# Kernel tuning notes

Measured on AMD Instinct MI355X. Metric: run time of the kernel, lower is better.

## Reference

```python
import jax, jax.numpy as jnp
import numpy as np

N = 16_777_216  # number of draft tokens / cache slots
ACCEPT_PROB = 0.7


def setup_inputs() -> dict:
    key = jax.random.key(0)
    k1, k2, k3 = jax.random.split(key, 3)
    idx = jax.random.randint(k1, (N,), 0, N, dtype=jnp.int64)
    keep = jax.random.uniform(k2, (N,)) < ACCEPT_PROB
    # rejected slots are marked -1, as in the original kernel
    accept_index = jnp.where(keep, idx, jnp.int64(-1))
    out_cache_loc = jax.random.normal(k3, (N,), dtype=jnp.float32)
    return {"accept_index": accept_index, "out_cache_loc": out_cache_loc}


def reference(accept_index, out_cache_loc):
    """Stream compaction: gather out_cache_loc[accept_index[i]] for every i with
    accept_index[i] >= 0, packed densely at the front of the output.

    The original returns an array of length num_accepted (data-dependent). For a
    static, jit-compatible shape we return a length-N array whose first
    num_accepted entries equal the original output and the rest are zero.
    """
    n = accept_index.shape[0]
    mask = accept_index >= 0                      # [N] bool
    # exclusive prefix sum of mask = destination slot for each accepted element
    dst = jnp.cumsum(mask.astype(jnp.int64)) - mask.astype(jnp.int64)  # [N]
    # gather (use 0 as a safe dummy index for rejected lanes)
    vals = out_cache_loc[jnp.where(mask, accept_index, 0)]             # [N]
    # scatter accepted values to their compacted slots; rejected lanes are
    # routed to index n, which mode='drop' discards
    scatter_idx = jnp.where(mask, dst, n)
    out = jnp.zeros((n,), dtype=out_cache_loc.dtype)
    out = out.at[scatter_idx].set(vals, mode="drop")
    return out
```

## Files before the change

kernel.cpp:

```cpp
#include <hip/hip_runtime.h>


#define N_TOTAL  16777216
#define BLOCK    256

#define EPT2     16
#define TILE2    (BLOCK * EPT2)
#define NB2      (N_TOTAL / TILE2)

#define SLICE_LG 20
#define SLICES   (N_TOTAL >> SLICE_LG)

typedef float vfloat4 __attribute__((ext_vector_type(4)));

__global__ __launch_bounds__(256) void k_init(unsigned long long* __restrict__ state) {
    state[blockIdx.x * 256 + threadIdx.x] = 0ULL;
}

__global__ __launch_bounds__(BLOCK) void k_compact(const int* __restrict__ idx,
                                                   const float* __restrict__ src,
                                                   float* __restrict__ out,
                                                   unsigned long long* __restrict__ state) {
    const int b = blockIdx.x;
    const int t = threadIdx.x;
    const int lane = t & 63, wave = t >> 6;

    const int4* p = (const int4*)(idx + (size_t)b * TILE2 + (size_t)t * EPT2);
    int v[EPT2];
#pragma unroll
    for (int j = 0; j < EPT2 / 4; ++j) {
        int4 q = p[j];
        v[4 * j + 0] = q.x; v[4 * j + 1] = q.y;
        v[4 * j + 2] = q.z; v[4 * j + 3] = q.w;
    }
    int cnt = 0;
#pragma unroll
    for (int j = 0; j < EPT2; ++j) cnt += (v[j] >= 0);

    int x = cnt;
#pragma unroll
    for (int d = 1; d < 64; d <<= 1) {
        int y = __shfl_up(x, d);
        if (lane >= d) x += y;
    }
    __shared__ int wsum[BLOCK / 64], woff[BLOCK / 64], btotal;
    __shared__ long long sBase;
    if (lane == 63) wsum[wave] = x;
    __syncthreads();
    if (t == 0) {
        int s = 0;
#pragma unroll
        for (int w = 0; w < BLOCK / 64; ++w) { woff[w] = s; s += wsum[w]; }
        btotal = s;
        if (b == 0) {
            __hip_atomic_store(&state[0], ((unsigned long long)s << 2) | 2ULL,
                               __ATOMIC_RELAXED, __HIP_MEMORY_SCOPE_AGENT);
            sBase = 0;
        } else {
            __hip_atomic_store(&state[b], ((unsigned long long)s << 2) | 1ULL,
                               __ATOMIC_RELAXED, __HIP_MEMORY_SCOPE_AGENT);
        }
    }

    if (b > 0 && wave == 0) {
        long long excl = 0;
        int look = b - 1;
        for (;;) {
            const int pos = look - lane;
            unsigned long long s = 2ULL;
            if (pos >= 0)
                s = __hip_atomic_load(&state[pos], __ATOMIC_RELAXED,
                                      __HIP_MEMORY_SCOPE_AGENT);
            for (;;) {
                const bool need = (pos >= 0) && ((s & 3ULL) == 0ULL);
                if (!__any(need)) break;
                if (need) {
                    __builtin_amdgcn_s_sleep(2);
                    s = __hip_atomic_load(&state[pos], __ATOMIC_RELAXED,
                                          __HIP_MEMORY_SCOPE_AGENT);
                }
            }
            const unsigned long long ball = __ballot((s & 3ULL) == 2ULL);
            const int fp = ball ? (__ffsll((long long)ball) - 1) : 64;
            long long c = (lane <= fp) ? (long long)(s >> 2) : 0;
#pragma unroll
            for (int d = 32; d; d >>= 1) c += __shfl_down(c, d);
            excl += __shfl(c, 0);
            if (ball) break;
            look -= 64;
        }
        if (lane == 0) {
            __hip_atomic_store(&state[b],
                               (((unsigned long long)(excl + btotal)) << 2) | 2ULL,
                               __ATOMIC_RELAXED, __HIP_MEMORY_SCOPE_AGENT);
            sBase = excl;
        }
    }
    __syncthreads();

    const int off0 = (x - cnt) + woff[wave];
    const int tot  = btotal;
    const long long base = sBase;

    __shared__ float vals[TILE2];
#pragma unroll 1
    for (int s = 0; s < SLICES; ++s) {
        float tmp[EPT2];
#pragma unroll
        for (int j = 0; j < EPT2; ++j) {
            const bool m = (int)((unsigned)v[j] >> SLICE_LG) == s;
            tmp[j] = src[m ? v[j] : 0];
        }
        asm volatile("s_waitcnt vmcnt(0)" ::: "memory");
        int o = off0;
#pragma unroll
        for (int j = 0; j < EPT2; ++j) {
            const bool acc = v[j] >= 0;
            const bool m = (int)((unsigned)v[j] >> SLICE_LG) == s;
            if (m) vals[o] = tmp[j];
            o += acc;
        }
    }
    __syncthreads();

    for (int i = t; i < tot; i += BLOCK)
        __builtin_nontemporal_store(vals[i], out + base + i);

    const long long rprev = (long long)b * TILE2 - base;
    const int rcnt = TILE2 - tot;
    float* zp = out + ((long long)N_TOTAL - rprev - rcnt);
    for (int i = t; i < rcnt; i += BLOCK)
        __builtin_nontemporal_store(0.0f, zp + i);
}

extern "C" void kernel_launch(void* const* d_in, const int* in_sizes, int n_in,
                              void* d_out, int out_size, void* d_ws, size_t ws_size,
                              hipStream_t stream) {
    const int*   idx = (const int*)d_in[0];
    const float* src = (const float*)d_in[1];
    float*       out = (float*)d_out;

    unsigned long long* state = (unsigned long long*)d_ws;

    k_init   <<<NB2 / 256, 256, 0, stream>>>(state);
    k_compact<<<NB2, BLOCK, 0, stream>>>(idx, src, out, state);
}
```

Before: 330.4 us.

## Persistent grid with per-tile gather before lookback and vectorized aligned stores

Launches a fixed grid of 2048 blocks that each process several tiles in generations, instead of one block per tile. Inside each tile the sliced gather now runs before the decoupled lookback, so waiting on predecessors overlaps with gather latency. It also adds nontemporal vector loads of indices, float4-aligned stores for the compacted and zero-fill regions, and an occupancy hint in the launch bounds. Persistent generations risk longer lookback chains and less latency hiding if occupancy is lower.

```diff
diff --git a/kernel.cpp b/kernel.cpp
--- a/kernel.cpp
+++ b/kernel.cpp
@@ -7,130 +7,169 @@
 #define EPT2     16
 #define TILE2    (BLOCK * EPT2)
 #define NB2      (N_TOTAL / TILE2)
+#define GRID     2048
+#define GENS     (NB2 / GRID)
 
 #define SLICE_LG 20
 #define SLICES   (N_TOTAL >> SLICE_LG)
 
 typedef float vfloat4 __attribute__((ext_vector_type(4)));
+typedef int   vint4   __attribute__((ext_vector_type(4)));
 
 __global__ __launch_bounds__(256) void k_init(unsigned long long* __restrict__ state) {
     state[blockIdx.x * 256 + threadIdx.x] = 0ULL;
 }
 
-__global__ __launch_bounds__(BLOCK) void k_compact(const int* __restrict__ idx,
-                                                   const float* __restrict__ src,
-                                                   float* __restrict__ out,
-                                                   unsigned long long* __restrict__ state) {
+__global__ __launch_bounds__(BLOCK, 8) void k_compact(const int* __restrict__ idx,
+                                                      const float* __restrict__ src,
+                                                      float* __restrict__ out,
+                                                      unsigned long long* __restrict__ state) {
     const int b = blockIdx.x;
     const int t = threadIdx.x;
     const int lane = t & 63, wave = t >> 6;
 
-    const int4* p = (const int4*)(idx + (size_t)b * TILE2 + (size_t)t * EPT2);
-    int v[EPT2];
-#pragma unroll
-    for (int j = 0; j < EPT2 / 4; ++j) {
-        int4 q = p[j];
-        v[4 * j + 0] = q.x; v[4 * j + 1] = q.y;
-        v[4 * j + 2] = q.z; v[4 * j + 3] = q.w;
-    }
-    int cnt = 0;
-#pragma unroll
-    for (int j = 0; j < EPT2; ++j) cnt += (v[j] >= 0);
-
-    int x = cnt;
-#pragma unroll
-    for (int d = 1; d < 64; d <<= 1) {
-        int y = __shfl_up(x, d);
-        if (lane >= d) x += y;
-    }
     __shared__ int wsum[BLOCK / 64], woff[BLOCK / 64], btotal;
     __shared__ long long sBase;
-    if (lane == 63) wsum[wave] = x;
-    __syncthreads();
-    if (t == 0) {
-        int s = 0;
+    __shared__ float vals[TILE2];
+
+    for (int gen = 0; gen < GENS; ++gen) {
+        const int tile = b + gen * GRID;
+
+        const vint4* p = (const vint4*)(idx + (size_t)tile * TILE2 + (size_t)t * EPT2);
+        int v[EPT2];
 #pragma unroll
-        for (int w = 0; w < BLOCK / 64; ++w) { woff[w] = s; s += wsum[w]; }
-        btotal = s;
-        if (b == 0) {
-            __hip_atomic_store(&state[0], ((unsigned long long)s << 2) | 2ULL,
-                               __ATOMIC_RELAXED, __HIP_MEMORY_SCOPE_AGENT);
-            sBase = 0;
-        } else {
-            __hip_atomic_store(&state[b], ((unsigned long long)s << 2) | 1ULL,
-                               __ATOMIC_RELAXED, __HIP_MEMORY_SCOPE_AGENT);
+        for (int j = 0; j < EPT2 / 4; ++j) {
+            vint4 q = __builtin_nontemporal_load(p + j);
+            v[4 * j + 0] = q.x; v[4 * j + 1] = q.y;
+            v[4 * j + 2] = q.z; v[4 * j + 3] = q.w;
         }
-    }
+        int cnt = 0;
+#pragma unroll
+        for (int j = 0; j < EPT2; ++j) cnt += (v[j] >= 0);
 
-    if (b > 0 && wave == 0) {
-        long long excl = 0;
-        int look = b - 1;
-        for (;;) {
-            const int pos = look - lane;
-            unsigned long long s = 2ULL;
-            if (pos >= 0)
-                s = __hip_atomic_load(&state[pos], __ATOMIC_RELAXED,
-                                      __HIP_MEMORY_SCOPE_AGENT);
+        int x = cnt;
+#pragma unroll
+        for (int d = 1; d < 64; d <<= 1) {
+            int y = __shfl_up(x, d);
+            if (lane >= d) x += y;
+        }
+        if (lane == 63) wsum[wave] = x;
+        __syncthreads();
+        if (t == 0) {
+            int s = 0;
+#pragma unroll
+            for (int w = 0; w < BLOCK / 64; ++w) { woff[w] = s; s += wsum[w]; }
+            btotal = s;
+            if (tile == 0) {
+                __hip_atomic_store(&state[0], ((unsigned long long)s << 2) | 2ULL,
+                                   __ATOMIC_RELAXED, __HIP_MEMORY_SCOPE_AGENT);
+                sBase = 0;
+            } else {
+                __hip_atomic_store(&state[tile], ((unsigned long long)s << 2) | 1ULL,
+                                   __ATOMIC_RELAXED, __HIP_MEMORY_SCOPE_AGENT);
+            }
+        }
+        __syncthreads();
+
+        const int off0 = (x - cnt) + woff[wave];
+
+#pragma unroll 1
+        for (int s = 0; s < SLICES; ++s) {
+            float tmp[EPT2];
+#pragma unroll
+            for (int j = 0; j < EPT2; ++j) {
+                const bool m = (int)((unsigned)v[j] >> SLICE_LG) == s;
+                tmp[j] = src[m ? v[j] : 0];
+            }
+            asm volatile("s_waitcnt vmcnt(0)" ::: "memory");
+            int o = off0;
+#pragma unroll
+            for (int j = 0; j < EPT2; ++j) {
+                const bool acc = v[j] >= 0;
+                const bool m = (int)((unsigned)v[j] >> SLICE_LG) == s;
+                if (m) vals[o] = tmp[j];
+                o += acc;
+            }
+        }
+
+        if (tile > 0 && wave == 0) {
+            long long excl = 0;
+            int look = tile - 1;
             for (;;) {
-                const bool need = (pos >= 0) && ((s & 3ULL) == 0ULL);
-                if (!__any(need)) break;
-                if (need) {
-                    __builtin_amdgcn_s_sleep(2);
+                const int pos = look - lane;
+                unsigned long long s = 2ULL;
+                if (pos >= 0)
                     s = __hip_atomic_load(&state[pos], __ATOMIC_RELAXED,
                                           __HIP_MEMORY_SCOPE_AGENT);
+                for (;;) {
+                    const bool need = (pos >= 0) && ((s & 3ULL) == 0ULL);
+                    if (!__any(need)) break;
+                    if (need) {
+                        __builtin_amdgcn_s_sleep(2);
+                        s = __hip_atomic_load(&state[pos], __ATOMIC_RELAXED,
+                                              __HIP_MEMORY_SCOPE_AGENT);
+                    }
                 }
+                const unsigned long long ball = __ballot((s & 3ULL) == 2ULL);
+                const int fp = ball ? (__ffsll((long long)ball) - 1) : 64;
+                long long c = (lane <= fp) ? (long long)(s >> 2) : 0;
+#pragma unroll
+                for (int d = 32; d; d >>= 1) c += __shfl_down(c, d);
+                excl += __shfl(c, 0);
+                if (ball) break;
+                look -= 64;
             }
-            const unsigned long long ball = __ballot((s & 3ULL) == 2ULL);
-            const int fp = ball ? (__ffsll((long long)ball) - 1) : 64;
-            long long c = (lane <= fp) ? (long long)(s >> 2) : 0;
-#pragma unroll
-            for (int d = 32; d; d >>= 1) c += __shfl_down(c, d);
-            excl += __shfl(c, 0);
-            if (ball) break;
-            look -= 64;
+            if (lane == 0) {
+                __hip_atomic_store(&state[tile],
+                                   (((unsigned long long)(excl + btotal)) << 2) | 2ULL,
+                                   __ATOMIC_RELAXED, __HIP_MEMORY_SCOPE_AGENT);
+                sBase = excl;
+            }
         }
-        if (lane == 0) {
-            __hip_atomic_store(&state[b],
-                               (((unsigned long long)(excl + btotal)) << 2) | 2ULL,
-                               __ATOMIC_RELAXED, __HIP_MEMORY_SCOPE_AGENT);
-            sBase = excl;
+        __syncthreads();
+
+        const int tot = btotal;
+        const long long base = sBase;
+
+        {
+            const long long gbeg = base, gend = base + tot;
+            const long long a0 = (gbeg + 3) & ~3LL;
+            const long long a1 = gend & ~3LL;
+            const long long hend = a0 < gend ? a0 : gend;
+            for (long long g = gbeg + t; g < hend; g += BLOCK)
+                __builtin_nontemporal_store(vals[(int)(g - gbeg)], out + g);
+            if (a0 < gend) {
+                for (long long g = a0 + (long long)t * 4; g < a1; g += (long long)BLOCK * 4) {
+                    const int l = (int)(g - gbeg);
+                    vfloat4 w = { vals[l], vals[l + 1], vals[l + 2], vals[l + 3] };
+                    __builtin_nontemporal_store(w, (vfloat4*)(out + g));
+                }
+                for (long long g = a1 + t; g < gend; g += BLOCK)
+                    __builtin_nontemporal_store(vals[(int)(g - gbeg)], out + g);
+            }
         }
+
+        {
+            const long long rprev = (long long)tile * TILE2 - base;
+            const int rcnt = TILE2 - tot;
+            const long long zbeg = (long long)N_TOTAL - rprev - rcnt;
+            const long long zend = (long long)N_TOTAL - rprev;
+            const long long a0 = (zbeg + 3) & ~3LL;
+            const long long a1 = zend & ~3LL;
+            const long long hend = a0 < zend ? a0 : zend;
+            for (long long g = zbeg + t; g < hend; g += BLOCK)
+                __builtin_nontemporal_store(0.0f, out + g);
+            if (a0 < zend) {
+                const vfloat4 z = (vfloat4)(0.f);
+                for (long long g = a0 + (long long)t * 4; g < a1; g += (long long)BLOCK * 4)
+                    __builtin_nontemporal_store(z, (vfloat4*)(out + g));
+                for (long long g = a1 + t; g < zend; g += BLOCK)
+                    __builtin_nontemporal_store(0.0f, out + g);
+            }
+        }
+
+        __syncthreads();
     }
-    __syncthreads();
-
-    const int off0 = (x - cnt) + woff[wave];
-    const int tot  = btotal;
-    const long long base = sBase;
-
-    __shared__ float vals[TILE2];
-#pragma unroll 1
-    for (int s = 0; s < SLICES; ++s) {
-        float tmp[EPT2];
-#pragma unroll
-        for (int j = 0; j < EPT2; ++j) {
-            const bool m = (int)((unsigned)v[j] >> SLICE_LG) == s;
-            tmp[j] = src[m ? v[j] : 0];
-        }
-        asm volatile("s_waitcnt vmcnt(0)" ::: "memory");
-        int o = off0;
-#pragma unroll
-        for (int j = 0; j < EPT2; ++j) {
-            const bool acc = v[j] >= 0;
-            const bool m = (int)((unsigned)v[j] >> SLICE_LG) == s;
-            if (m) vals[o] = tmp[j];
-            o += acc;
-        }
-    }
-    __syncthreads();
-
-    for (int i = t; i < tot; i += BLOCK)
-        __builtin_nontemporal_store(vals[i], out + base + i);
-
-    const long long rprev = (long long)b * TILE2 - base;
-    const int rcnt = TILE2 - tot;
-    float* zp = out + ((long long)N_TOTAL - rprev - rcnt);
-    for (int i = t; i < rcnt; i += BLOCK)
-        __builtin_nontemporal_store(0.0f, zp + i);
 }
 
 extern "C" void kernel_launch(void* const* d_in, const int* in_sizes, int n_in,
@@ -143,5 +182,5 @@
     unsigned long long* state = (unsigned long long*)d_ws;
 
     k_init   <<<NB2 / 256, 256, 0, stream>>>(state);
-    k_compact<<<NB2, BLOCK, 0, stream>>>(idx, src, out, state);
+    k_compact<<<GRID, BLOCK, 0, stream>>>(idx, src, out, state);
 }
```

Result: no change. 328.3 us (-0.6%).
